# Kernel optimization log

Measured on AMD Instinct MI355X. Metric: run time of the kernel, lower is better.

The kernel has to match this reference:

```python
import jax, jax.numpy as jnp
import numpy as np

NUM_HEADS = 8
KERNEL = 7
LOW_RANK = 4


def setup_inputs() -> dict:
    key = jax.random.key(0)
    ks = jax.random.split(key, 10)
    B, H, W, C = 4, 56, 56, 256
    nh, K, lr = NUM_HEADS, KERNEL, LOW_RANK
    s = 0.02
    return {
        "x": jax.random.normal(ks[0], (B, H, W, C), jnp.float32),
        "Wq": jax.random.normal(ks[1], (C, nh * lr), jnp.float32) * s,
        "bq": jnp.zeros((nh * lr,), jnp.float32),
        "Wk": jax.random.normal(ks[2], (C, nh * lr), jnp.float32) * s,
        "bk": jnp.zeros((nh * lr,), jnp.float32),
        "Wv": jax.random.normal(ks[3], (C, C), jnp.float32) * s,
        "bv": jnp.zeros((C,), jnp.float32),
        "rpb": jax.random.normal(ks[4], (nh, 2 * K - 1, 2 * K - 1), jnp.float32) * s,
        "Wp": jax.random.normal(ks[5], (C, C), jnp.float32) * s,
        "bp": jnp.zeros((C,), jnp.float32),
    }


def reference(x, Wq, bq, Wk, bk, Wv, bv, rpb, Wp, bp):
    B, H, W, C = x.shape
    nh, K, lr = NUM_HEADS, KERNEL, LOW_RANK
    hd = C // nh
    r = K // 2
    scale = hd ** -0.5

    # Projections. Note: the original uses a raw reshape (B,H,W,nh*lr)->(B,nh,H,W,lr),
    # which we replicate exactly (row-major reshape, no permute).
    q = (x @ Wq + bq).reshape(B, nh, H, W, lr) * scale
    k = (x @ Wk + bk).reshape(B, nh, H, W, lr)
    v = (x @ Wv + bv).reshape(B, nh, H, W, hd)

    # NATTEN window start indices (clamped so each query sees exactly K keys per axis).
    start_h = jnp.clip(jnp.arange(H) - r, 0, H - K)  # (H,)
    start_w = jnp.clip(jnp.arange(W) - r, 0, W - K)  # (W,)
    idx_h = start_h[:, None] + jnp.arange(K)[None, :]  # (H, K)
    idx_w = start_w[:, None] + jnp.arange(K)[None, :]  # (W, K)

    # Gather local K/V windows: (B, nh, H, K, W, K, d)
    k_win = k[:, :, idx_h][:, :, :, :, idx_w]
    v_win = v[:, :, idx_h][:, :, :, :, idx_w]

    # Scores: (B, nh, H, W, K, K)
    attn = jnp.einsum('bhijc,bhikjlc->bhijkl', q, k_win)

    # Relative position bias indices: (key_pos - query_pos) + (K-1)
    bi = idx_h - jnp.arange(H)[:, None] + (K - 1)  # (H, K)
    bj = idx_w - jnp.arange(W)[:, None] + (K - 1)  # (W, K)
    bias = rpb[:, bi][:, :, :, bj]                 # (nh, H, K, W, K)
    attn = attn + bias.transpose(0, 1, 3, 2, 4)[None]  # (B, nh, H, W, K, K)

    attn = jax.nn.softmax(attn.reshape(B, nh, H, W, K * K), axis=-1)
    attn = attn.reshape(B, nh, H, W, K, K)

    # Weighted aggregation of V windows: (B, nh, H, W, hd)
    out = jnp.einsum('bhijkl,bhikjld->bhijd', attn, v_win)
    out = out.transpose(0, 2, 3, 1, 4).reshape(B, H, W, C)
    return out @ Wp + bp
```

## Files before the change

kernel.cpp:

```cpp
#include <hip/hip_runtime.h>
#include <hip/hip_bf16.h>

#define BD 4
#define HD_ 56
#define WD 56
#define CD 256
#define NH 8
#define KW 7
#define LR 4
#define HDIM 32
#define MB (HD_*WD)
#define NROWS (BD*MB)
#define QK_PER_B (HD_*WD*32)
#define V_PER_B  (HD_*WD*256)

typedef short short8 __attribute__((ext_vector_type(8)));
typedef float floatx4 __attribute__((ext_vector_type(4)));

static __device__ inline ushort f2bf(float f) {
    __hip_bfloat16 h = __float2bfloat16(f);
    return *(ushort*)&h;
}
static __device__ inline float bf2f(uint h16) {
    union { uint u; float f; } c; c.u = h16 << 16; return c.f;
}
static __device__ inline float bf2f_hi(uint u) {
    union { uint v; float f; } c; c.v = u & 0xffff0000u; return c.f;
}

__global__ __launch_bounds__(256) void prep_w(
    const float* __restrict__ Wq, const float* __restrict__ Wk,
    const float* __restrict__ Wv, const float* __restrict__ bq,
    const float* __restrict__ bk, const float* __restrict__ bv,
    const float* __restrict__ Wp,
    ushort* __restrict__ WpkT, ushort* __restrict__ WpT, float* __restrict__ pb)
{
    int idx = blockIdx.x * 256 + threadIdx.x;
    if (idx < 81920) {
        int n = idx >> 8, k = idx & 255;
        float v;
        if (n < 32)       v = Wq[k * 32 + n];
        else if (n < 64)  v = Wk[k * 32 + (n - 32)];
        else              v = Wv[k * 256 + (n - 64)];
        WpkT[idx] = f2bf(v);
    } else if (idx < 81920 + 65536) {
        int j = idx - 81920;
        int n = j >> 8, k = j & 255;
        WpT[j] = f2bf(Wp[k * 256 + n]);
    } else if (idx < 81920 + 65536 + 320) {
        int n = idx - (81920 + 65536);
        pb[n] = (n < 32) ? bq[n] : (n < 64) ? bk[n - 32] : bv[n - 64];
    }
}

__global__ __launch_bounds__(256) void mfma_qkv(
    const float* __restrict__ X, const ushort* __restrict__ Bt,
    const float* __restrict__ pb, ushort* __restrict__ Qb,
    ushort* __restrict__ Kb, ushort* __restrict__ Vb)
{
    __shared__ ushort As[64 * 40];
    __shared__ ushort Bs[64 * 40];

    const int t = threadIdx.x;
    const int m0 = blockIdx.y * 64;
    const int n0 = blockIdx.x * 64;
    const int r  = t >> 2;
    const int kq = (t & 3) << 3;
    const int lane = t & 63, w = t >> 6;
    const int col = lane & 15, quad = lane >> 4;
    const int q8 = quad << 3;

    floatx4 acc[4] = {{0,0,0,0},{0,0,0,0},{0,0,0,0},{0,0,0,0}};

    for (int k0 = 0; k0 < 256; k0 += 32) {
        float4 a0 = *(const float4*)&X[(m0 + r) * 256 + k0 + kq];
        float4 a1 = *(const float4*)&X[(m0 + r) * 256 + k0 + kq + 4];
        uint4 bv = *(const uint4*)&Bt[(n0 + r) * 256 + k0 + kq];
        union { ushort h[8]; uint4 u; } pa;
        pa.h[0] = f2bf(a0.x); pa.h[1] = f2bf(a0.y); pa.h[2] = f2bf(a0.z); pa.h[3] = f2bf(a0.w);
        pa.h[4] = f2bf(a1.x); pa.h[5] = f2bf(a1.y); pa.h[6] = f2bf(a1.z); pa.h[7] = f2bf(a1.w);
        __syncthreads();
        *(uint4*)&As[r * 40 + kq] = pa.u;
        *(uint4*)&Bs[r * 40 + kq] = bv;
        __syncthreads();
        short8 af = *(short8*)&As[((w << 4) + col) * 40 + q8];
#pragma unroll
        for (int nt = 0; nt < 4; ++nt) {
            short8 bf = *(short8*)&Bs[((nt << 4) + col) * 40 + q8];
            acc[nt] = __builtin_amdgcn_mfma_f32_16x16x32_bf16(af, bf, acc[nt], 0, 0, 0);
        }
    }

#pragma unroll
    for (int nt = 0; nt < 4; ++nt) {
        int gn = n0 + (nt << 4) + col;
        float bias = pb[gn];
#pragma unroll
        for (int rg = 0; rg < 4; ++rg) {
            int m = m0 + (w << 4) + (quad << 2) + rg;
            ushort h = f2bf(acc[nt][rg] + bias);
            if (n0 == 0 && nt < 2)      Qb[m * 32 + gn] = h;
            else if (n0 == 0)           Kb[m * 32 + (gn - 32)] = h;
            else                        Vb[m * 256 + (gn - 64)] = h;
        }
    }
}

__global__ __launch_bounds__(256) void mfma_out(
    const ushort* __restrict__ Ag, const ushort* __restrict__ Bt,
    const float* __restrict__ bp, float* __restrict__ out)
{
    __shared__ ushort As[64 * 40];
    __shared__ ushort Bs[64 * 40];

    const int t = threadIdx.x;
    const int m0 = blockIdx.y * 64;
    const int n0 = blockIdx.x * 64;
    const int r  = t >> 2;
    const int kq = (t & 3) << 3;
    const int lane = t & 63, w = t >> 6;
    const int col = lane & 15, quad = lane >> 4;
    const int q8 = quad << 3;

    floatx4 acc[4] = {{0,0,0,0},{0,0,0,0},{0,0,0,0},{0,0,0,0}};

    for (int k0 = 0; k0 < 256; k0 += 32) {
        uint4 av = *(const uint4*)&Ag[(m0 + r) * 256 + k0 + kq];
        uint4 bv = *(const uint4*)&Bt[(n0 + r) * 256 + k0 + kq];
        __syncthreads();
        *(uint4*)&As[r * 40 + kq] = av;
        *(uint4*)&Bs[r * 40 + kq] = bv;
        __syncthreads();
        short8 af = *(short8*)&As[((w << 4) + col) * 40 + q8];
#pragma unroll
        for (int nt = 0; nt < 4; ++nt) {
            short8 bf = *(short8*)&Bs[((nt << 4) + col) * 40 + q8];
            acc[nt] = __builtin_amdgcn_mfma_f32_16x16x32_bf16(af, bf, acc[nt], 0, 0, 0);
        }
    }

#pragma unroll
    for (int nt = 0; nt < 4; ++nt) {
        int gn = n0 + (nt << 4) + col;
        float bias = bp[gn];
#pragma unroll
        for (int rg = 0; rg < 4; ++rg) {
            int m = m0 + (w << 4) + (quad << 2) + rg;
            out[m * 256 + gn] = acc[nt][rg] + bias;
        }
    }
}

__global__ __launch_bounds__(256, 8) void natten_attn_t(
    const ushort* __restrict__ Qb, const ushort* __restrict__ Kb,
    const ushort* __restrict__ Vb, const float* __restrict__ rpb,
    ushort* __restrict__ Ab)
{
    __shared__ ushort Ks[196 * 4];
    __shared__ ushort Vs[4 * 196 * 8];
    __shared__ float  Rs[169];

    const int tj = blockIdx.x, ti = blockIdx.y;
    const int n = blockIdx.z & 7, b = blockIdx.z >> 3;
    const int t = threadIdx.x;
    const int i0 = ti * 8, j0 = tj * 8;
    const int rs = min(max(i0 - 3, 0), HD_ - 14);
    const int cs = min(max(j0 - 3, 0), WD - 14);

    const ushort* kb = Kb + b * QK_PER_B + n * (HD_ * WD * LR);
    const ushort* vb = Vb + b * V_PER_B + n * (HD_ * WD * HDIM);

    if (t < 196) {
        int r = t / 14, c = t % 14;
        *(uint2*)&Ks[t * 4] = *(const uint2*)&kb[(rs + r) * (WD * LR) + (cs + c) * LR];
    }
    if (t < 169) Rs[t] = rpb[n * 169 + t];
    for (int idx = t; idx < 784; idx += 256) {
        int oct = idx & 3, pos = idx >> 2;
        int r = pos / 14, c = pos % 14;
        *(uint4*)&Vs[(oct * 196 + pos) * 8] =
            *(const uint4*)&vb[(rs + r) * (WD * HDIM) + (cs + c) * HDIM + oct * 8];
    }
    __syncthreads();

    const int q  = t >> 2, p = t & 3;
    const int qi = q >> 3, qj = q & 7;
    const int i = i0 + qi, j = j0 + qj;
    const int sh = min(max(i - 3, 0), HD_ - KW);
    const int sw = min(max(j - 3, 0), WD - KW);
    const int oh = sh - rs, ow = sw - cs;

    union { uint2 u; uint w[2]; } qr;
    qr.u = *(const uint2*)&Qb[b * QK_PER_B + n * (HD_ * WD * LR) + i * (WD * LR) + j * LR];
    const float scale = 0.17677669529663687f;
    float qx = bf2f(qr.w[0] & 0xffff) * scale, qy = bf2f_hi(qr.w[0]) * scale;
    float qz = bf2f(qr.w[1] & 0xffff) * scale, qw = bf2f_hi(qr.w[1]) * scale;

    const int rb0 = (sh - i + 6) * 13 + (sw - j + 6);

    float sum = 0.f;
    float a[8] = {0.f, 0.f, 0.f, 0.f, 0.f, 0.f, 0.f, 0.f};
    const ushort* vsl = &Vs[p * (196 * 8)];
    for (int kh = 0; kh < KW; ++kh) {
        int kpos  = (oh + kh) * 14 + ow;
        int rbase = rb0 + kh * 13;
#pragma unroll
        for (int kw = 0; kw < KW; ++kw) {
            union { uint2 u; uint w[2]; } kr;
            kr.u = *(const uint2*)&Ks[(kpos + kw) * 4];
            float d = Rs[rbase + kw];
            d = fmaf(qx, bf2f(kr.w[0] & 0xffff), d);
            d = fmaf(qy, bf2f_hi(kr.w[0]), d);
            d = fmaf(qz, bf2f(kr.w[1] & 0xffff), d);
            d = fmaf(qw, bf2f_hi(kr.w[1]), d);
            float e = __expf(d);
            sum += e;
            union { uint4 u; uint w[4]; } vr;
            vr.u = *(const uint4*)&vsl[(kpos + kw) * 8];
#pragma unroll
            for (int c = 0; c < 4; ++c) {
                a[2 * c]     = fmaf(e, bf2f(vr.w[c] & 0xffff), a[2 * c]);
                a[2 * c + 1] = fmaf(e, bf2f_hi(vr.w[c]),       a[2 * c + 1]);
            }
        }
    }
    float inv = 1.0f / sum;

    union { ushort h[8]; uint4 u; } pk;
#pragma unroll
    for (int c = 0; c < 8; ++c) pk.h[c] = f2bf(a[c] * inv);
    *(uint4*)&Ab[(((b * HD_ + i) * WD + j)) * CD + n * HDIM + p * 8] = pk.u;
}

extern "C" void kernel_launch(void* const* d_in, const int* in_sizes, int n_in,
                              void* d_out, int out_size, void* d_ws, size_t ws_size,
                              hipStream_t stream) {
    const float* x   = (const float*)d_in[0];
    const float* Wq  = (const float*)d_in[1];
    const float* bq  = (const float*)d_in[2];
    const float* Wk  = (const float*)d_in[3];
    const float* bk  = (const float*)d_in[4];
    const float* Wv  = (const float*)d_in[5];
    const float* bv  = (const float*)d_in[6];
    const float* rpb = (const float*)d_in[7];
    const float* Wp  = (const float*)d_in[8];
    const float* bp  = (const float*)d_in[9];
    float* out = (float*)d_out;

    ushort* WpkT = (ushort*)d_ws;
    ushort* WpT  = WpkT + 81920;
    ushort* Ab   = WpT + 65536;
    ushort* Qb   = Ab + 3211264;
    ushort* Kb   = Qb + BD * QK_PER_B;
    ushort* Vb   = Kb + BD * QK_PER_B;
    float*  pb   = (float*)(Vb + BD * V_PER_B);

    prep_w<<<(81920 + 65536 + 320 + 255) / 256, 256, 0, stream>>>(
        Wq, Wk, Wv, bq, bk, bv, Wp, WpkT, WpT, pb);

    mfma_qkv<<<dim3(5, NROWS / 64), 256, 0, stream>>>(x, WpkT, pb, Qb, Kb, Vb);

    natten_attn_t<<<dim3(7, 7, 32), 256, 0, stream>>>(Qb, Kb, Vb, rpb, Ab);

    mfma_out<<<dim3(4, NROWS / 64), 256, 0, stream>>>(Ab, WpT, bp, out);
}
```

Measured before the change: 119.9 us.

## Enlarge GEMM M-tile to 128 rows and pre-convert attention K/V tiles to fp32 in LDS

Both projection GEMMs now compute 128x64 output tiles per block, with each wave handling two 16-row sub-tiles. Each B fragment loaded from LDS is reused across twice as many rows and the grid is halved. Separately, the attention kernel converts the K and V window tiles to fp32 once while staging them into shared memory, with padded rows, so the inner 49-tap loop no longer repeats bf16 unpacking. The cost is double the LDS footprint for K/V, which may reduce occupancy, and more accumulator registers in the GEMMs.

```diff
diff --git a/kernel.cpp b/kernel.cpp
--- a/kernel.cpp
+++ b/kernel.cpp
@@ -58,50 +58,63 @@
     const float* __restrict__ pb, ushort* __restrict__ Qb,
     ushort* __restrict__ Kb, ushort* __restrict__ Vb)
 {
-    __shared__ ushort As[64 * 40];
+    __shared__ ushort As[128 * 40];
     __shared__ ushort Bs[64 * 40];
 
     const int t = threadIdx.x;
-    const int m0 = blockIdx.y * 64;
+    const int m0 = blockIdx.y * 128;
     const int n0 = blockIdx.x * 64;
-    const int r  = t >> 2;
-    const int kq = (t & 3) << 3;
+    const int ar = t >> 1;
+    const int ac = (t & 1) << 4;
+    const int br = t >> 2;
+    const int bc = (t & 3) << 3;
     const int lane = t & 63, w = t >> 6;
     const int col = lane & 15, quad = lane >> 4;
     const int q8 = quad << 3;
 
-    floatx4 acc[4] = {{0,0,0,0},{0,0,0,0},{0,0,0,0},{0,0,0,0}};
+    floatx4 acc[2][4] = {};
 
     for (int k0 = 0; k0 < 256; k0 += 32) {
-        float4 a0 = *(const float4*)&X[(m0 + r) * 256 + k0 + kq];
-        float4 a1 = *(const float4*)&X[(m0 + r) * 256 + k0 + kq + 4];
-        uint4 bv = *(const uint4*)&Bt[(n0 + r) * 256 + k0 + kq];
-        union { ushort h[8]; uint4 u; } pa;
-        pa.h[0] = f2bf(a0.x); pa.h[1] = f2bf(a0.y); pa.h[2] = f2bf(a0.z); pa.h[3] = f2bf(a0.w);
-        pa.h[4] = f2bf(a1.x); pa.h[5] = f2bf(a1.y); pa.h[6] = f2bf(a1.z); pa.h[7] = f2bf(a1.w);
-        __syncthreads();
-        *(uint4*)&As[r * 40 + kq] = pa.u;
-        *(uint4*)&Bs[r * 40 + kq] = bv;
-        __syncthreads();
-        short8 af = *(short8*)&As[((w << 4) + col) * 40 + q8];
+        float4 a0 = *(const float4*)&X[(m0 + ar) * 256 + k0 + ac];
+        float4 a1 = *(const float4*)&X[(m0 + ar) * 256 + k0 + ac + 4];
+        float4 a2 = *(const float4*)&X[(m0 + ar) * 256 + k0 + ac + 8];
+        float4 a3 = *(const float4*)&X[(m0 + ar) * 256 + k0 + ac + 12];
+        uint4 bv = *(const uint4*)&Bt[(n0 + br) * 256 + k0 + bc];
+        union { ushort h[8]; uint4 u; } p0, p1;
+        p0.h[0] = f2bf(a0.x); p0.h[1] = f2bf(a0.y); p0.h[2] = f2bf(a0.z); p0.h[3] = f2bf(a0.w);
+        p0.h[4] = f2bf(a1.x); p0.h[5] = f2bf(a1.y); p0.h[6] = f2bf(a1.z); p0.h[7] = f2bf(a1.w);
+        p1.h[0] = f2bf(a2.x); p1.h[1] = f2bf(a2.y); p1.h[2] = f2bf(a2.z); p1.h[3] = f2bf(a2.w);
+        p1.h[4] = f2bf(a3.x); p1.h[5] = f2bf(a3.y); p1.h[6] = f2bf(a3.z); p1.h[7] = f2bf(a3.w);
+        __syncthreads();
+        *(uint4*)&As[ar * 40 + ac]     = p0.u;
+        *(uint4*)&As[ar * 40 + ac + 8] = p1.u;
+        *(uint4*)&Bs[br * 40 + bc]     = bv;
+        __syncthreads();
+#pragma unroll
+        for (int s = 0; s < 2; ++s) {
+            short8 af = *(short8*)&As[((w << 5) + (s << 4) + col) * 40 + q8];
+#pragma unroll
+            for (int nt = 0; nt < 4; ++nt) {
+                short8 bf = *(short8*)&Bs[((nt << 4) + col) * 40 + q8];
+                acc[s][nt] = __builtin_amdgcn_mfma_f32_16x16x32_bf16(af, bf, acc[s][nt], 0, 0, 0);
+            }
+        }
+    }
+
+#pragma unroll
+    for (int s = 0; s < 2; ++s) {
 #pragma unroll
         for (int nt = 0; nt < 4; ++nt) {
-            short8 bf = *(short8*)&Bs[((nt << 4) + col) * 40 + q8];
-            acc[nt] = __builtin_amdgcn_mfma_f32_16x16x32_bf16(af, bf, acc[nt], 0, 0, 0);
-        }
-    }
-
-#pragma unroll
-    for (int nt = 0; nt < 4; ++nt) {
-        int gn = n0 + (nt << 4) + col;
-        float bias = pb[gn];
-#pragma unroll
-        for (int rg = 0; rg < 4; ++rg) {
-            int m = m0 + (w << 4) + (quad << 2) + rg;
-            ushort h = f2bf(acc[nt][rg] + bias);
-            if (n0 == 0 && nt < 2)      Qb[m * 32 + gn] = h;
-            else if (n0 == 0)           Kb[m * 32 + (gn - 32)] = h;
-            else                        Vb[m * 256 + (gn - 64)] = h;
+            int gn = n0 + (nt << 4) + col;
+            float bias = pb[gn];
+#pragma unroll
+            for (int rg = 0; rg < 4; ++rg) {
+                int m = m0 + (w << 5) + (s << 4) + (quad << 2) + rg;
+                ushort h = f2bf(acc[s][nt][rg] + bias);
+                if (n0 == 0 && nt < 2)      Qb[m * 32 + gn] = h;
+                else if (n0 == 0)           Kb[m * 32 + (gn - 32)] = h;
+                else                        Vb[m * 256 + (gn - 64)] = h;
+            }
         }
     }
 }
@@ -110,43 +123,53 @@
     const ushort* __restrict__ Ag, const ushort* __restrict__ Bt,
     const float* __restrict__ bp, float* __restrict__ out)
 {
-    __shared__ ushort As[64 * 40];
+    __shared__ ushort As[128 * 40];
     __shared__ ushort Bs[64 * 40];
 
     const int t = threadIdx.x;
-    const int m0 = blockIdx.y * 64;
+    const int m0 = blockIdx.y * 128;
     const int n0 = blockIdx.x * 64;
-    const int r  = t >> 2;
-    const int kq = (t & 3) << 3;
+    const int ar = t >> 1;
+    const int ac = (t & 1) << 4;
+    const int br = t >> 2;
+    const int bc = (t & 3) << 3;
     const int lane = t & 63, w = t >> 6;
     const int col = lane & 15, quad = lane >> 4;
     const int q8 = quad << 3;
 
-    floatx4 acc[4] = {{0,0,0,0},{0,0,0,0},{0,0,0,0},{0,0,0,0}};
+    floatx4 acc[2][4] = {};
 
     for (int k0 = 0; k0 < 256; k0 += 32) {
-        uint4 av = *(const uint4*)&Ag[(m0 + r) * 256 + k0 + kq];
-        uint4 bv = *(const uint4*)&Bt[(n0 + r) * 256 + k0 + kq];
-        __syncthreads();
-        *(uint4*)&As[r * 40 + kq] = av;
-        *(uint4*)&Bs[r * 40 + kq] = bv;
-        __syncthreads();
-        short8 af = *(short8*)&As[((w << 4) + col) * 40 + q8];
+        uint4 av0 = *(const uint4*)&Ag[(m0 + ar) * 256 + k0 + ac];
+        uint4 av1 = *(const uint4*)&Ag[(m0 + ar) * 256 + k0 + ac + 8];
+        uint4 bv  = *(const uint4*)&Bt[(n0 + br) * 256 + k0 + bc];
+        __syncthreads();
+        *(uint4*)&As[ar * 40 + ac]     = av0;
+        *(uint4*)&As[ar * 40 + ac + 8] = av1;
+        *(uint4*)&Bs[br * 40 + bc]     = bv;
+        __syncthreads();
+#pragma unroll
+        for (int s = 0; s < 2; ++s) {
+            short8 af = *(short8*)&As[((w << 5) + (s << 4) + col) * 40 + q8];
+#pragma unroll
+            for (int nt = 0; nt < 4; ++nt) {
+                short8 bf = *(short8*)&Bs[((nt << 4) + col) * 40 + q8];
+                acc[s][nt] = __builtin_amdgcn_mfma_f32_16x16x32_bf16(af, bf, acc[s][nt], 0, 0, 0);
+            }
+        }
+    }
+
+#pragma unroll
+    for (int s = 0; s < 2; ++s) {
 #pragma unroll
         for (int nt = 0; nt < 4; ++nt) {
-            short8 bf = *(short8*)&Bs[((nt << 4) + col) * 40 + q8];
-            acc[nt] = __builtin_amdgcn_mfma_f32_16x16x32_bf16(af, bf, acc[nt], 0, 0, 0);
-        }
-    }
-
-#pragma unroll
-    for (int nt = 0; nt < 4; ++nt) {
-        int gn = n0 + (nt << 4) + col;
-        float bias = bp[gn];
-#pragma unroll
-        for (int rg = 0; rg < 4; ++rg) {
-            int m = m0 + (w << 4) + (quad << 2) + rg;
-            out[m * 256 + gn] = acc[nt][rg] + bias;
+            int gn = n0 + (nt << 4) + col;
+            float bias = bp[gn];
+#pragma unroll
+            for (int rg = 0; rg < 4; ++rg) {
+                int m = m0 + (w << 5) + (s << 4) + (quad << 2) + rg;
+                out[m * 256 + gn] = acc[s][nt][rg] + bias;
+            }
         }
     }
 }
@@ -156,8 +179,8 @@
     const ushort* __restrict__ Vb, const float* __restrict__ rpb,
     ushort* __restrict__ Ab)
 {
-    __shared__ ushort Ks[196 * 4];
-    __shared__ ushort Vs[4 * 196 * 8];
+    __shared__ float4 Ksf[196];
+    __shared__ float4 Vsf[8 * 197];
     __shared__ float  Rs[169];
 
     const int tj = blockIdx.x, ti = blockIdx.y;
@@ -172,14 +195,23 @@
 
     if (t < 196) {
         int r = t / 14, c = t % 14;
-        *(uint2*)&Ks[t * 4] = *(const uint2*)&kb[(rs + r) * (WD * LR) + (cs + c) * LR];
+        union { uint2 u; uint w[2]; } kr;
+        kr.u = *(const uint2*)&kb[(rs + r) * (WD * LR) + (cs + c) * LR];
+        Ksf[t] = make_float4(bf2f(kr.w[0] & 0xffff), bf2f_hi(kr.w[0]),
+                             bf2f(kr.w[1] & 0xffff), bf2f_hi(kr.w[1]));
     }
     if (t < 169) Rs[t] = rpb[n * 169 + t];
     for (int idx = t; idx < 784; idx += 256) {
         int oct = idx & 3, pos = idx >> 2;
         int r = pos / 14, c = pos % 14;
-        *(uint4*)&Vs[(oct * 196 + pos) * 8] =
-            *(const uint4*)&vb[(rs + r) * (WD * HDIM) + (cs + c) * HDIM + oct * 8];
+        union { uint4 u; uint w[4]; } vr;
+        vr.u = *(const uint4*)&vb[(rs + r) * (WD * HDIM) + (cs + c) * HDIM + oct * 8];
+        Vsf[(2 * oct) * 197 + pos] =
+            make_float4(bf2f(vr.w[0] & 0xffff), bf2f_hi(vr.w[0]),
+                        bf2f(vr.w[1] & 0xffff), bf2f_hi(vr.w[1]));
+        Vsf[(2 * oct + 1) * 197 + pos] =
+            make_float4(bf2f(vr.w[2] & 0xffff), bf2f_hi(vr.w[2]),
+                        bf2f(vr.w[3] & 0xffff), bf2f_hi(vr.w[3]));
     }
     __syncthreads();
 
@@ -200,28 +232,27 @@
 
     float sum = 0.f;
     float a[8] = {0.f, 0.f, 0.f, 0.f, 0.f, 0.f, 0.f, 0.f};
-    const ushort* vsl = &Vs[p * (196 * 8)];
+    const float4* v0 = &Vsf[(2 * p) * 197];
+    const float4* v1 = &Vsf[(2 * p + 1) * 197];
     for (int kh = 0; kh < KW; ++kh) {
         int kpos  = (oh + kh) * 14 + ow;
         int rbase = rb0 + kh * 13;
 #pragma unroll
         for (int kw = 0; kw < KW; ++kw) {
-            union { uint2 u; uint w[2]; } kr;
-            kr.u = *(const uint2*)&Ks[(kpos + kw) * 4];
+            float4 kf = Ksf[kpos + kw];
             float d = Rs[rbase + kw];
-            d = fmaf(qx, bf2f(kr.w[0] & 0xffff), d);
-            d = fmaf(qy, bf2f_hi(kr.w[0]), d);
-            d = fmaf(qz, bf2f(kr.w[1] & 0xffff), d);
-            d = fmaf(qw, bf2f_hi(kr.w[1]), d);
+            d = fmaf(qx, kf.x, d);
+            d = fmaf(qy, kf.y, d);
+            d = fmaf(qz, kf.z, d);
+            d = fmaf(qw, kf.w, d);
             float e = __expf(d);
             sum += e;
-            union { uint4 u; uint w[4]; } vr;
-            vr.u = *(const uint4*)&vsl[(kpos + kw) * 8];
-#pragma unroll
-            for (int c = 0; c < 4; ++c) {
-                a[2 * c]     = fmaf(e, bf2f(vr.w[c] & 0xffff), a[2 * c]);
-                a[2 * c + 1] = fmaf(e, bf2f_hi(vr.w[c]),       a[2 * c + 1]);
-            }
+            float4 x0 = v0[kpos + kw];
+            float4 x1 = v1[kpos + kw];
+            a[0] = fmaf(e, x0.x, a[0]); a[1] = fmaf(e, x0.y, a[1]);
+            a[2] = fmaf(e, x0.z, a[2]); a[3] = fmaf(e, x0.w, a[3]);
+            a[4] = fmaf(e, x1.x, a[4]); a[5] = fmaf(e, x1.y, a[5]);
+            a[6] = fmaf(e, x1.z, a[6]); a[7] = fmaf(e, x1.w, a[7]);
         }
     }
     float inv = 1.0f / sum;
@@ -258,9 +289,9 @@
     prep_w<<<(81920 + 65536 + 320 + 255) / 256, 256, 0, stream>>>(
         Wq, Wk, Wv, bq, bk, bv, Wp, WpkT, WpT, pb);
 
-    mfma_qkv<<<dim3(5, NROWS / 64), 256, 0, stream>>>(x, WpkT, pb, Qb, Kb, Vb);
+    mfma_qkv<<<dim3(5, NROWS / 128), 256, 0, stream>>>(x, WpkT, pb, Qb, Kb, Vb);
 
     natten_attn_t<<<dim3(7, 7, 32), 256, 0, stream>>>(Qb, Kb, Vb, rpb, Ab);
 
-    mfma_out<<<dim3(4, NROWS / 64), 256, 0, stream>>>(Ab, WpT, bp, out);
-}
+    mfma_out<<<dim3(4, NROWS / 128), 256, 0, stream>>>(Ab, WpT, bp, out);
+}
```

Result: no change. 120.4 us, median of 2 (+0.4%).
